# Performance work log

Measured on AMD Instinct MI355X. Metric: run time of the kernel, lower is better.

Reference implementation:

```python
import jax, jax.numpy as jnp
import numpy as np

N, C, H = 4096, 768, 12
HD = C // H
SCALE = HD ** -0.5


def setup_inputs() -> dict:
    key = jax.random.key(0)
    k1, k2, k3 = jax.random.split(key, 3)
    x = jax.random.normal(k1, (N, C), dtype=jnp.float32)
    w_qkv = jax.random.normal(k2, (C, 3 * C), dtype=jnp.float32) * (C ** -0.5)
    w_proj = jax.random.normal(k3, (C, C), dtype=jnp.float32) * (C ** -0.5)
    b_proj = jnp.zeros((C,), dtype=jnp.float32)
    return {"x": x, "w_qkv": w_qkv, "w_proj": w_proj, "b_proj": b_proj}


def reference(x, w_qkv, w_proj, b_proj):
    n, c = x.shape
    # fused QKV projection (qkv_bias=False): [N, 3C] -> [3, H, N, hd]
    qkv = (x @ w_qkv).reshape(n, 3, H, HD)
    qkv = jnp.transpose(qkv, (1, 2, 0, 3))  # (3, H, N, hd)
    q, k, v = qkv[0], qkv[1], qkv[2]
    # scaled dot-product attention per head: (H, N, N)
    attn = jnp.einsum('hnd,hmd->hnm', q, k) * SCALE
    attn = jax.nn.softmax(attn, axis=-1)
    # attn_drop is identity (rate=0, eval mode)
    out = jnp.einsum('hnm,hmd->hnd', attn, v)          # (H, N, hd)
    out = jnp.transpose(out, (1, 0, 2)).reshape(n, c)  # (N, C)
    # output projection (bias by default in nn.Dense); proj_drop identity
    return out @ w_proj + b_proj
```

## Files before the change

### kernel.cpp

```cpp
#include <hip/hip_runtime.h>

#define N_TOK 4096
#define C_DIM 768
#define H_NUM 12
#define QKV_N 2304

typedef __attribute__((ext_vector_type(8))) short bf16x8;
typedef __attribute__((ext_vector_type(4))) float f32x4;
typedef __attribute__((ext_vector_type(16))) float f32x16;
typedef __attribute__((ext_vector_type(4))) unsigned int u32x4;

static __device__ __forceinline__ unsigned short f2bf(float f) {
  unsigned u = __builtin_bit_cast(unsigned, f);
  u += 0x7FFF + ((u >> 16) & 1);
  return (unsigned short)(u >> 16);
}

static __device__ __forceinline__ float exp2_fast(float x) {
  float r; asm("v_exp_f32 %0, %1" : "=v"(r) : "v"(x)); return r;
}

#define GLOAD_LDS16(g, l)                                                     \
  __builtin_amdgcn_global_load_lds(                                           \
      (const __attribute__((address_space(1))) void*)(g),                     \
      (__attribute__((address_space(3))) void*)(l), 16, 0, 0)

#define Q_SCALE 0.18033688011112042f

__global__ __launch_bounds__(256) void conv_bf16(
    const float* __restrict__ in, unsigned short* __restrict__ out, int n8) {
  const int i = blockIdx.x * 256 + threadIdx.x;
  if (i >= n8) return;
  const float4 a = reinterpret_cast<const float4*>(in)[i * 2];
  const float4 b = reinterpret_cast<const float4*>(in)[i * 2 + 1];
  unsigned short tmp[8] = {f2bf(a.x), f2bf(a.y), f2bf(a.z), f2bf(a.w),
                           f2bf(b.x), f2bf(b.y), f2bf(b.z), f2bf(b.w)};
  reinterpret_cast<bf16x8*>(out)[i] = *reinterpret_cast<bf16x8*>(tmp);
}

__global__ __launch_bounds__(256) void transpose_cvt(
    const float* __restrict__ in, unsigned short* __restrict__ out,
    int K, int N) {
  __shared__ unsigned short T[64][65];
  const int t = threadIdx.x;
  const int k0 = blockIdx.y * 64, n0 = blockIdx.x * 64;
  {
    const int r = t >> 2, qd = t & 3;
#pragma unroll
    for (int i = 0; i < 4; ++i) {
      const int c = qd * 16 + i * 4;
      const float4 v = *reinterpret_cast<const float4*>(
          &in[(size_t)(k0 + r) * N + n0 + c]);
      T[r][c + 0] = f2bf(v.x); T[r][c + 1] = f2bf(v.y);
      T[r][c + 2] = f2bf(v.z); T[r][c + 3] = f2bf(v.w);
    }
  }
  __syncthreads();
#pragma unroll
  for (int i = 0; i < 2; ++i) {
    const int cid = t + i * 256;
    const int rn = cid >> 3, cx = cid & 7;
    unsigned short tmp[8];
#pragma unroll
    for (int j = 0; j < 8; ++j) tmp[j] = T[cx * 8 + j][rn];
    *reinterpret_cast<bf16x8*>(&out[(size_t)(n0 + rn) * K + k0 + cx * 8]) =
        *reinterpret_cast<bf16x8*>(tmp);
  }
}

__global__ __launch_bounds__(256) void gemm_qkv_bf16(
    const unsigned short* __restrict__ A, const unsigned short* __restrict__ Bt,
    unsigned short* __restrict__ qw, unsigned short* __restrict__ kw,
    unsigned short* __restrict__ vw) {
  __shared__ unsigned short As[128 * 32];
  __shared__ unsigned short Bs[128 * 32];
  const int t = threadIdx.x;
  const int lane = t & 63, wid = t >> 6;
  const int lr = lane & 15, lg = lane >> 4;
  const int m_base = blockIdx.y * 128, n_base = blockIdx.x * 128;
  const int wm = (wid >> 1) * 64, wn = (wid & 1) * 64;
  const int c_row = lane >> 2;
  const int c_col = (lane & 3) * 8;

  f32x4 acc[4][4];
#pragma unroll
  for (int mt = 0; mt < 4; ++mt)
#pragma unroll
    for (int nt = 0; nt < 4; ++nt) acc[mt][nt] = (f32x4){0.f, 0.f, 0.f, 0.f};

  for (int kt = 0; kt < 24; ++kt) {
    const int k0 = kt * 32;
    __syncthreads();
#pragma unroll
    for (int i = 0; i < 2; ++i) {
      const int ch = wid * 2 + i;
      GLOAD_LDS16(&A[(size_t)(m_base + ch * 16 + c_row) * 768 + k0 + c_col],
                  &As[ch * 512]);
      GLOAD_LDS16(&Bt[(size_t)(n_base + ch * 16 + c_row) * 768 + k0 + c_col],
                  &Bs[ch * 512]);
    }
    __syncthreads();
    bf16x8 af[4], bfr[4];
#pragma unroll
    for (int mt = 0; mt < 4; ++mt)
      af[mt] = *reinterpret_cast<const bf16x8*>(&As[(wm + mt * 16 + lr) * 32 + lg * 8]);
#pragma unroll
    for (int nt = 0; nt < 4; ++nt)
      bfr[nt] = *reinterpret_cast<const bf16x8*>(&Bs[(wn + nt * 16 + lr) * 32 + lg * 8]);
#pragma unroll
    for (int mt = 0; mt < 4; ++mt)
#pragma unroll
      for (int nt = 0; nt < 4; ++nt)
        acc[mt][nt] = __builtin_amdgcn_mfma_f32_16x16x32_bf16(af[mt], bfr[nt],
                                                              acc[mt][nt], 0, 0, 0);
  }
#pragma unroll
  for (int mt = 0; mt < 4; ++mt)
#pragma unroll
    for (int nt = 0; nt < 4; ++nt)
#pragma unroll
      for (int r = 0; r < 4; ++r) {
        const int m = m_base + wm + mt * 16 + lg * 4 + r;
        const int c = n_base + wn + nt * 16 + lr;
        const float v = acc[mt][nt][r];
        const int which = c / 768;
        const int cc = c - which * 768;
        const int h = cc >> 6, d = cc & 63;
        if (which == 0) {
          qw[((size_t)h * N_TOK + m) * 64 + d] = f2bf(v * Q_SCALE);
        } else if (which == 1) {
          kw[((size_t)h * N_TOK + m) * 64 + d] = f2bf(v);
        } else {
          vw[((size_t)h * 64 + d) * N_TOK + m] = f2bf(v);
        }
      }
}

__global__ __launch_bounds__(256) void gemm_proj_bf16(
    const unsigned short* __restrict__ A, const unsigned short* __restrict__ Bt,
    const float* __restrict__ bias, float* __restrict__ out) {
  __shared__ unsigned short As[128 * 32];
  __shared__ unsigned short Bs[128 * 32];
  const int t = threadIdx.x;
  const int lane = t & 63, wid = t >> 6;
  const int lr = lane & 15, lg = lane >> 4;
  const int m_base = blockIdx.y * 128, n_base = blockIdx.x * 128;
  const int wm = (wid >> 1) * 64, wn = (wid & 1) * 64;
  const int c_row = lane >> 2;
  const int c_col = (lane & 3) * 8;

  f32x4 acc[4][4];
#pragma unroll
  for (int mt = 0; mt < 4; ++mt)
#pragma unroll
    for (int nt = 0; nt < 4; ++nt) acc[mt][nt] = (f32x4){0.f, 0.f, 0.f, 0.f};

  for (int kt = 0; kt < 24; ++kt) {
    const int k0 = kt * 32;
    __syncthreads();
#pragma unroll
    for (int i = 0; i < 2; ++i) {
      const int ch = wid * 2 + i;
      GLOAD_LDS16(&A[(size_t)(m_base + ch * 16 + c_row) * 768 + k0 + c_col],
                  &As[ch * 512]);
      GLOAD_LDS16(&Bt[(size_t)(n_base + ch * 16 + c_row) * 768 + k0 + c_col],
                  &Bs[ch * 512]);
    }
    __syncthreads();
    bf16x8 af[4], bfr[4];
#pragma unroll
    for (int mt = 0; mt < 4; ++mt)
      af[mt] = *reinterpret_cast<const bf16x8*>(&As[(wm + mt * 16 + lr) * 32 + lg * 8]);
#pragma unroll
    for (int nt = 0; nt < 4; ++nt)
      bfr[nt] = *reinterpret_cast<const bf16x8*>(&Bs[(wn + nt * 16 + lr) * 32 + lg * 8]);
#pragma unroll
    for (int mt = 0; mt < 4; ++mt)
#pragma unroll
      for (int nt = 0; nt < 4; ++nt)
        acc[mt][nt] = __builtin_amdgcn_mfma_f32_16x16x32_bf16(af[mt], bfr[nt],
                                                              acc[mt][nt], 0, 0, 0);
  }
#pragma unroll
  for (int nt = 0; nt < 4; ++nt) {
    const int n = n_base + wn + nt * 16 + lr;
    const float bv = bias[n];
#pragma unroll
    for (int mt = 0; mt < 4; ++mt)
#pragma unroll
      for (int r = 0; r < 4; ++r) {
        const int m = m_base + wm + mt * 16 + lg * 4 + r;
        out[(size_t)m * 768 + n] = acc[mt][nt][r] + bv;
      }
  }
}

__global__ __launch_bounds__(256) void attn_kernel(
    const unsigned short* __restrict__ qw, const unsigned short* __restrict__ kw,
    const unsigned short* __restrict__ vw, unsigned short* __restrict__ ow) {
  __shared__ unsigned short smem[18432];
  const int t = threadIdx.x;
  const int lane = t & 63;
  const int wid = t >> 6;
  const int qsub = wid & 1;
  const int kvh = wid >> 1;
  const int q31 = lane & 31;
  const int hi = lane >> 5;
  const int swz = (blockIdx.x & 7) * 96 + (blockIdx.x >> 3);
  const int h = swz >> 6;
  const int qt = swz & 63;
  const int q0 = qt * 64 + qsub * 32;

  unsigned short* Ks = &smem[kvh * 9216];
  unsigned short* Vs = Ks + 4608;

  const unsigned short* kbase = &kw[(size_t)h * N_TOK * 64];
  const unsigned short* vbase = &vw[(size_t)h * 64 * N_TOK];
  const int kv0 = kvh * 2048;

  bf16x8 qf[4];
#pragma unroll
  for (int ks = 0; ks < 4; ++ks)
    qf[ks] = *reinterpret_cast<const bf16x8*>(
        &qw[((size_t)h * N_TOK + q0 + q31) * 64 + ks * 16 + hi * 8]);

  f32x16 acc0, acc1;
#pragma unroll
  for (int r = 0; r < 16; ++r) { acc0[r] = 0.f; acc1[r] = 0.f; }
  float l_run = 0.f;

  const int tg = t & 127;
  const int srow = tg >> 3;
  const int sseg = (tg & 7) * 8;

  bf16x8 kst[4], vst[4];
#pragma unroll
  for (int i = 0; i < 4; ++i) {
    const int row = srow + i * 16;
    kst[i] = *reinterpret_cast<const bf16x8*>(&kbase[(size_t)(kv0 + row) * 64 + sseg]);
    vst[i] = *reinterpret_cast<const bf16x8*>(&vbase[(size_t)row * N_TOK + kv0 + sseg]);
  }

  for (int kvt = 0; kvt < 32; ++kvt) {
    const int kv = kv0 + kvt * 64;
    __syncthreads();
#pragma unroll
    for (int i = 0; i < 4; ++i) {
      const int row = srow + i * 16;
      *reinterpret_cast<bf16x8*>(&Ks[row * 72 + sseg]) = kst[i];
      *reinterpret_cast<bf16x8*>(&Vs[row * 72 + sseg]) = vst[i];
    }
    __syncthreads();
    const int kvn = (kvt + 1 < 32) ? kv + 64 : kv0;
#pragma unroll
    for (int i = 0; i < 4; ++i) {
      const int row = srow + i * 16;
      kst[i] = *reinterpret_cast<const bf16x8*>(&kbase[(size_t)(kvn + row) * 64 + sseg]);
      vst[i] = *reinterpret_cast<const bf16x8*>(&vbase[(size_t)row * N_TOK + kvn + sseg]);
    }

#pragma unroll
    for (int ct = 0; ct < 2; ++ct) {
      f32x16 s;
#pragma unroll
      for (int r = 0; r < 16; ++r) s[r] = 0.f;
      __builtin_amdgcn_s_setprio(1);
#pragma unroll
      for (int ks = 0; ks < 4; ++ks) {
        const bf16x8 kf = *reinterpret_cast<const bf16x8*>(
            &Ks[(ct * 32 + q31) * 72 + ks * 16 + hi * 8]);
        s = __builtin_amdgcn_mfma_f32_32x32x16_bf16(kf, qf[ks], s, 0, 0, 0);
      }
      __builtin_amdgcn_s_setprio(0);

      float p[16];
#pragma unroll
      for (int r = 0; r < 16; ++r) p[r] = exp2_fast(s[r]);
      float s8[8];
#pragma unroll
      for (int r = 0; r < 8; ++r) s8[r] = p[r] + p[r + 8];
#pragma unroll
      for (int r = 0; r < 4; ++r) s8[r] = s8[r] + s8[r + 4];
      float rs = (s8[0] + s8[1]) + (s8[2] + s8[3]);
      rs += __shfl_xor(rs, 32);
      l_run += rs;

      unsigned dw[8];
#pragma unroll
      for (int m2 = 0; m2 < 8; ++m2)
        asm("v_cvt_pk_bf16_f32 %0, %1, %2"
            : "=v"(dw[m2]) : "v"(p[2 * m2]), "v"(p[2 * m2 + 1]));
      asm("v_permlane32_swap_b32 %0, %1" : "+v"(dw[0]), "+v"(dw[2]));
      asm("v_permlane32_swap_b32 %0, %1" : "+v"(dw[1]), "+v"(dw[3]));
      asm("v_permlane32_swap_b32 %0, %1" : "+v"(dw[4]), "+v"(dw[6]));
      asm("v_permlane32_swap_b32 %0, %1" : "+v"(dw[5]), "+v"(dw[7]));

      __builtin_amdgcn_s_setprio(1);
#pragma unroll
      for (int ksl = 0; ksl < 2; ++ksl) {
        u32x4 u;
        u.x = dw[ksl * 4 + 0]; u.y = dw[ksl * 4 + 1];
        u.z = dw[ksl * 4 + 2]; u.w = dw[ksl * 4 + 3];
        const bf16x8 pa = __builtin_bit_cast(bf16x8, u);
        const int kg = ct * 2 + ksl;
        const bf16x8 vf0 = *reinterpret_cast<const bf16x8*>(
            &Vs[q31 * 72 + kg * 16 + hi * 8]);
        const bf16x8 vf1 = *reinterpret_cast<const bf16x8*>(
            &Vs[(32 + q31) * 72 + kg * 16 + hi * 8]);
        acc0 = __builtin_amdgcn_mfma_f32_32x32x16_bf16(pa, vf0, acc0, 0, 0, 0);
        acc1 = __builtin_amdgcn_mfma_f32_32x32x16_bf16(pa, vf1, acc1, 0, 0, 0);
      }
      __builtin_amdgcn_s_setprio(0);
    }
  }

  __syncthreads();
  float* ex = reinterpret_cast<float*>(smem) + qsub * 2304;
  if (kvh == 1) {
    float* pdst = ex + lane * 36;
#pragma unroll
    for (int r = 0; r < 16; ++r) { pdst[r] = acc0[r]; pdst[16 + r] = acc1[r]; }
    pdst[32] = l_run;
  }
  __syncthreads();
  if (kvh == 0) {
    const float* psrc = ex + lane * 36;
    const float linv = 1.0f / (l_run + psrc[32]);
#pragma unroll
    for (int r = 0; r < 16; ++r) {
      const int crow = (r & 3) + 8 * (r >> 2) + 4 * hi;
      const float iv = __shfl(linv, crow);
      const size_t base = (size_t)(q0 + crow) * C_DIM + h * 64;
      ow[base + q31] = f2bf((acc0[r] + psrc[r]) * iv);
      ow[base + 32 + q31] = f2bf((acc1[r] + psrc[16 + r]) * iv);
    }
  }
}

extern "C" void kernel_launch(void* const* d_in, const int* in_sizes, int n_in,
                              void* d_out, int out_size, void* d_ws, size_t ws_size,
                              hipStream_t stream) {
  (void)in_sizes; (void)n_in; (void)out_size; (void)ws_size;
  const float* x = (const float*)d_in[0];
  const float* w_qkv = (const float*)d_in[1];
  const float* w_proj = (const float*)d_in[2];
  const float* b_proj = (const float*)d_in[3];
  float* out = (float*)d_out;

  const size_t HNd = (size_t)H_NUM * N_TOK * 64;
  unsigned short* qw = (unsigned short*)d_ws;
  unsigned short* kw = qw + HNd;
  unsigned short* vw = kw + HNd;
  unsigned short* xb = vw + HNd;
  unsigned short* ow = xb;
  unsigned short* wT = xb + HNd;
  unsigned short* wqkvT = wT;
  unsigned short* wprojT = wT;

  conv_bf16<<<dim3((N_TOK * C_DIM / 8 + 255) / 256), 256, 0, stream>>>(
      x, xb, N_TOK * C_DIM / 8);
  transpose_cvt<<<dim3(QKV_N / 64, C_DIM / 64), 256, 0, stream>>>(
      w_qkv, wqkvT, C_DIM, QKV_N);
  gemm_qkv_bf16<<<dim3(QKV_N / 128, N_TOK / 128), 256, 0, stream>>>(
      xb, wqkvT, qw, kw, vw);
  transpose_cvt<<<dim3(C_DIM / 64, C_DIM / 64), 256, 0, stream>>>(
      w_proj, wprojT, C_DIM, C_DIM);
  attn_kernel<<<dim3(768), 256, 0, stream>>>(qw, kw, vw, ow);
  gemm_proj_bf16<<<dim3(C_DIM / 128, N_TOK / 128), 256, 0, stream>>>(
      ow, wprojT, b_proj, out);
}
```

Before: 153.1 us.

## Double-buffer attention K/V tiles and swizzle GEMM block order

The attention kernel now keeps two K/V tiles in LDS and writes the next tile into the idle buffer while computing on the current one. This cuts the barriers per iteration from two to one. The per-tile cross-half row-sum shuffle is replaced by a single shuffle after the loop. Both GEMMs remap block indices with an XCD-aware swizzle to improve L2 locality. LDS use per attention block doubles, which may reduce occupancy.

New measurement: 153.3 us. About the same (+0.1%).

```diff
diff --git a/kernel.cpp b/kernel.cpp
--- a/kernel.cpp
+++ b/kernel.cpp
@@ -77,7 +77,9 @@
   const int t = threadIdx.x;
   const int lane = t & 63, wid = t >> 6;
   const int lr = lane & 15, lg = lane >> 4;
-  const int m_base = blockIdx.y * 128, n_base = blockIdx.x * 128;
+  const int lid = blockIdx.y * 18 + blockIdx.x;
+  const int swz = (lid & 7) * 72 + (lid >> 3);
+  const int m_base = (swz / 18) * 128, n_base = (swz % 18) * 128;
   const int wm = (wid >> 1) * 64, wn = (wid & 1) * 64;
   const int c_row = lane >> 2;
   const int c_col = (lane & 3) * 8;
@@ -144,7 +146,9 @@
   const int t = threadIdx.x;
   const int lane = t & 63, wid = t >> 6;
   const int lr = lane & 15, lg = lane >> 4;
-  const int m_base = blockIdx.y * 128, n_base = blockIdx.x * 128;
+  const int lid = blockIdx.y * 6 + blockIdx.x;
+  const int swz = (lid & 7) * 24 + (lid >> 3);
+  const int m_base = (swz / 6) * 128, n_base = (swz % 6) * 128;
   const int wm = (wid >> 1) * 64, wn = (wid & 1) * 64;
   const int c_row = lane >> 2;
   const int c_col = (lane & 3) * 8;
@@ -198,7 +202,7 @@
 __global__ __launch_bounds__(256) void attn_kernel(
     const unsigned short* __restrict__ qw, const unsigned short* __restrict__ kw,
     const unsigned short* __restrict__ vw, unsigned short* __restrict__ ow) {
-  __shared__ unsigned short smem[18432];
+  __shared__ unsigned short smem[36864];
   const int t = threadIdx.x;
   const int lane = t & 63;
   const int wid = t >> 6;
@@ -211,8 +215,7 @@
   const int qt = swz & 63;
   const int q0 = qt * 64 + qsub * 32;
 
-  unsigned short* Ks = &smem[kvh * 9216];
-  unsigned short* Vs = Ks + 4608;
+  unsigned short* gbase = &smem[kvh * 18432];
 
   const unsigned short* kbase = &kw[(size_t)h * N_TOK * 64];
   const unsigned short* vbase = &vw[(size_t)h * 64 * N_TOK];
@@ -240,24 +243,26 @@
     kst[i] = *reinterpret_cast<const bf16x8*>(&kbase[(size_t)(kv0 + row) * 64 + sseg]);
     vst[i] = *reinterpret_cast<const bf16x8*>(&vbase[(size_t)row * N_TOK + kv0 + sseg]);
   }
-
+#pragma unroll
+  for (int i = 0; i < 4; ++i) {
+    const int row = srow + i * 16;
+    *reinterpret_cast<bf16x8*>(&gbase[row * 72 + sseg]) = kst[i];
+    *reinterpret_cast<bf16x8*>(&gbase[4608 + row * 72 + sseg]) = vst[i];
+  }
+#pragma unroll
+  for (int i = 0; i < 4; ++i) {
+    const int row = srow + i * 16;
+    kst[i] = *reinterpret_cast<const bf16x8*>(
+        &kbase[(size_t)(kv0 + 64 + row) * 64 + sseg]);
+    vst[i] = *reinterpret_cast<const bf16x8*>(
+        &vbase[(size_t)row * N_TOK + kv0 + 64 + sseg]);
+  }
+  __syncthreads();
+
+  int cur = 0;
   for (int kvt = 0; kvt < 32; ++kvt) {
-    const int kv = kv0 + kvt * 64;
-    __syncthreads();
-#pragma unroll
-    for (int i = 0; i < 4; ++i) {
-      const int row = srow + i * 16;
-      *reinterpret_cast<bf16x8*>(&Ks[row * 72 + sseg]) = kst[i];
-      *reinterpret_cast<bf16x8*>(&Vs[row * 72 + sseg]) = vst[i];
-    }
-    __syncthreads();
-    const int kvn = (kvt + 1 < 32) ? kv + 64 : kv0;
-#pragma unroll
-    for (int i = 0; i < 4; ++i) {
-      const int row = srow + i * 16;
-      kst[i] = *reinterpret_cast<const bf16x8*>(&kbase[(size_t)(kvn + row) * 64 + sseg]);
-      vst[i] = *reinterpret_cast<const bf16x8*>(&vbase[(size_t)row * N_TOK + kvn + sseg]);
-    }
+    const unsigned short* Ks = gbase + cur * 9216;
+    const unsigned short* Vs = Ks + 4608;
 
 #pragma unroll
     for (int ct = 0; ct < 2; ++ct) {
@@ -281,9 +286,7 @@
       for (int r = 0; r < 8; ++r) s8[r] = p[r] + p[r + 8];
 #pragma unroll
       for (int r = 0; r < 4; ++r) s8[r] = s8[r] + s8[r + 4];
-      float rs = (s8[0] + s8[1]) + (s8[2] + s8[3]);
-      rs += __shfl_xor(rs, 32);
-      l_run += rs;
+      l_run += (s8[0] + s8[1]) + (s8[2] + s8[3]);
 
       unsigned dw[8];
 #pragma unroll
@@ -312,7 +315,32 @@
       }
       __builtin_amdgcn_s_setprio(0);
     }
-  }
+
+    if (kvt + 1 < 32) {
+      unsigned short* nK = gbase + (cur ^ 1) * 9216;
+#pragma unroll
+      for (int i = 0; i < 4; ++i) {
+        const int row = srow + i * 16;
+        *reinterpret_cast<bf16x8*>(&nK[row * 72 + sseg]) = kst[i];
+        *reinterpret_cast<bf16x8*>(&nK[4608 + row * 72 + sseg]) = vst[i];
+      }
+      if (kvt + 2 < 32) {
+        const int kvn = kv0 + (kvt + 2) * 64;
+#pragma unroll
+        for (int i = 0; i < 4; ++i) {
+          const int row = srow + i * 16;
+          kst[i] = *reinterpret_cast<const bf16x8*>(
+              &kbase[(size_t)(kvn + row) * 64 + sseg]);
+          vst[i] = *reinterpret_cast<const bf16x8*>(
+              &vbase[(size_t)row * N_TOK + kvn + sseg]);
+        }
+      }
+    }
+    __syncthreads();
+    cur ^= 1;
+  }
+
+  l_run += __shfl_xor(l_run, 32);
 
   __syncthreads();
   float* ex = reinterpret_cast<float*>(smem) + qsub * 2304;
```
